# Kernel optimization log

Measured on AMD Instinct MI355X. Metric: run time of the kernel, lower is better.

The kernel has to match this reference:

```python
import jax, jax.numpy as jnp
import numpy as np

# ---- fixed wavelet filters (Selesnick FSfarras first-stage + Kingsbury Q-shift) ----
_F1 = np.array([
    [0.0, 0.0],
    [-0.08838834764832, -0.01122679215254],
    [0.08838834764832, 0.01122679215254],
    [0.69587998903400, 0.08838834764832],
    [0.69587998903400, 0.08838834764832],
    [0.08838834764832, -0.69587998903400],
    [-0.08838834764832, 0.69587998903400],
    [0.01122679215254, -0.08838834764832],
    [0.01122679215254, -0.08838834764832],
    [0.0, 0.0]], np.float32)
_F2 = np.array([
    [0.01122679215254, 0.0],
    [0.01122679215254, 0.0],
    [-0.08838834764832, -0.08838834764832],
    [0.08838834764832, -0.08838834764832],
    [0.69587998903400, 0.69587998903400],
    [0.69587998903400, -0.69587998903400],
    [0.08838834764832, 0.08838834764832],
    [-0.08838834764832, 0.08838834764832],
    [0.0, 0.01122679215254],
    [0.0, -0.01122679215254]], np.float32)
_Q1 = np.array([
    [0.03516384, 0.0],
    [0.0, 0.0],
    [-0.08832942, -0.11430184],
    [0.23389032, 0.0],
    [0.76027237, 0.58751830],
    [0.58751830, -0.76027237],
    [0.0, 0.23389032],
    [-0.11430184, 0.08832942],
    [0.0, 0.0],
    [0.0, -0.03516384]], np.float32)
_Q2 = np.array([
    [0.0, -0.03516384],
    [0.0, 0.0],
    [-0.11430184, 0.08832942],
    [0.0, 0.23389032],
    [0.58751830, -0.76027237],
    [0.76027237, 0.58751830],
    [0.23389032, 0.0],
    [-0.08832942, -0.11430184],
    [0.0, 0.0],
    [0.03516384, 0.0]], np.float32)
# synthesis filters are the time-reversed analysis filters
FSF = jnp.asarray(np.stack([_F1[::-1].copy(), _F2[::-1].copy()]))  # [2, 10, 2] first stage
SF = jnp.asarray(np.stack([_Q1[::-1].copy(), _Q2[::-1].copy()]))   # [2, 10, 2] Q-shift


def _upconv(x, f, axis):
    """Upsample-by-2 + full convolution with 1D filter f along `axis` (upfirdn(x,f,2,1))."""
    L = f.shape[0]
    xm = jnp.moveaxis(x, axis, -1)
    shp = xm.shape
    xr = xm.reshape(-1, 1, shp[-1])  # [M, 1, n] NCW
    k = f[::-1].astype(x.dtype).reshape(1, 1, L)  # flip -> true convolution
    y = jax.lax.conv_general_dilated(
        xr, k, window_strides=(1,), padding=[(L - 1, L - 1)],
        lhs_dilation=(2,), dimension_numbers=('NCW', 'OIW', 'NCW'))  # [M,1,2n+L-2]
    y = y.reshape(shp[:-1] + (y.shape[-1],))
    return jnp.moveaxis(y, -1, axis)


def sfb1d(lo, hi, sf, axis):
    """1D synthesis filter bank with periodic wrap + circular shift (Selesnick sfb1D)."""
    L = sf.shape[0]
    N = 2 * lo.shape[axis]
    y = _upconv(lo, sf[:, 0], axis) + _upconv(hi, sf[:, 1], axis)  # length N+L-2
    yN = jax.lax.slice_in_dim(y, 0, N, axis=axis)
    tail = jax.lax.slice_in_dim(y, N, N + L - 2, axis=axis)
    head = jax.lax.slice_in_dim(yN, 0, L - 2, axis=axis) + tail
    rest = jax.lax.slice_in_dim(yN, L - 2, N, axis=axis)
    return jnp.roll(jnp.concatenate([head, rest], axis=axis), 1 - L // 2, axis=axis)


def sfb2d(lo, hi3, sf_row, sf_col):
    """2D separable synthesis: hi3 = (LH, HL, HH); x is [B, H, W, C]."""
    lo = sfb1d(lo, hi3[0], sf_col, axis=2)
    h = sfb1d(hi3[1], hi3[2], sf_col, axis=2)
    return sfb1d(lo, h, sf_row, axis=1)


def _idtcwt(highs0, highs1, lows):
    inv_sqrt2 = jnp.asarray(1.0 / np.sqrt(2.0), highs0.dtype)

    def pm(a, b):
        return (a + b) * inv_sqrt2, (a - b) * inv_sqrt2

    # orientation butterflies per level (add_sub)
    wi = [[[[None] * 3 for _ in range(2)] for _ in range(2)] for _ in range(2)]
    for j, hj in enumerate((highs0, highs1)):
        for b in range(3):
            u, v = pm(hj[0, 0, b], hj[1, 1, b])
            wi[j][0][0][b], wi[j][1][1][b] = u, v
            u, v = pm(hj[0, 1, b], hj[1, 0, b])
            wi[j][0][1][b], wi[j][1][0][b] = u, v

    y = jnp.zeros_like(lows[0, 0], shape=(lows.shape[2], lows.shape[3] * 4,
                                          lows.shape[4] * 4, lows.shape[5]))
    for m in range(2):
        for n in range(2):
            lo = lows[m, n]
            lo = sfb2d(lo, wi[1][m][n], SF[m], SF[n])      # level 2 (Q-shift)
            lo = sfb2d(lo, wi[0][m][n], FSF[m], FSF[n])    # level 1 (first stage)
            y = y + lo
    return y / 2


def setup_inputs() -> dict:
    key = jax.random.key(0)
    k0, k1, k2 = jax.random.split(key, 3)
    B, C = 16, 3
    highs0 = jax.random.normal(k0, (2, 2, 3, B, 256, 256, C), dtype=jnp.float32)
    highs1 = jax.random.normal(k1, (2, 2, 3, B, 128, 128, C), dtype=jnp.float32)
    lows = jax.random.normal(k2, (2, 2, B, 128, 128, C), dtype=jnp.float32)
    return {"highs0": highs0, "highs1": highs1, "lows": lows}


def reference(highs0, highs1, lows):
    return _idtcwt(highs0, highs1, lows)
```

## Files before the change

### kernel.cpp

```cpp
#include <hip/hip_runtime.h>

#define INV_SQRT2 0.70710678118654752440f

__constant__ float c_first[2][10][2] = {
  { { 0.00000000000000f,  0.00000000000000f},
    {-0.08838834764832f, -0.01122679215254f},
    { 0.08838834764832f,  0.01122679215254f},
    { 0.69587998903400f,  0.08838834764832f},
    { 0.69587998903400f,  0.08838834764832f},
    { 0.08838834764832f, -0.69587998903400f},
    {-0.08838834764832f,  0.69587998903400f},
    { 0.01122679215254f, -0.08838834764832f},
    { 0.01122679215254f, -0.08838834764832f},
    { 0.00000000000000f,  0.00000000000000f} },
  { { 0.01122679215254f,  0.00000000000000f},
    { 0.01122679215254f,  0.00000000000000f},
    {-0.08838834764832f, -0.08838834764832f},
    { 0.08838834764832f, -0.08838834764832f},
    { 0.69587998903400f,  0.69587998903400f},
    { 0.69587998903400f, -0.69587998903400f},
    { 0.08838834764832f,  0.08838834764832f},
    {-0.08838834764832f,  0.08838834764832f},
    { 0.00000000000000f,  0.01122679215254f},
    { 0.00000000000000f, -0.01122679215254f} }
};

__constant__ float c_qshift[2][10][2] = {
  { { 0.03516384f,  0.00000000f},
    { 0.00000000f,  0.00000000f},
    {-0.08832942f, -0.11430184f},
    { 0.23389032f,  0.00000000f},
    { 0.76027237f,  0.58751830f},
    { 0.58751830f, -0.76027237f},
    { 0.00000000f,  0.23389032f},
    {-0.11430184f,  0.08832942f},
    { 0.00000000f,  0.00000000f},
    { 0.00000000f, -0.03516384f} },
  { { 0.00000000f, -0.03516384f},
    { 0.00000000f,  0.00000000f},
    {-0.11430184f,  0.08832942f},
    { 0.00000000f,  0.23389032f},
    { 0.58751830f, -0.76027237f},
    { 0.76027237f,  0.58751830f},
    { 0.23389032f,  0.00000000f},
    {-0.08832942f, -0.11430184f},
    { 0.00000000f,  0.00000000f},
    { 0.03516384f,  0.00000000f} }
};

__global__ __launch_bounds__(128) void idtcwt_stage1(
    const float* __restrict__ lows, const float* __restrict__ highs1,
    float* __restrict__ lo2)
{
  constexpr int HIN = 128, WIN = 128, C = 3, B = 16;
  constexpr int ROWF  = WIN * C;
  constexpr int ROWO  = 2 * WIN * C;
  constexpr int PLANE = HIN * WIN * C;
  constexpr int SEG   = 16;

  const int jj = blockIdx.x * 128 + threadIdx.x;
  const int c  = jj % 3;
  const int t  = jj / 3;
  const int z  = blockIdx.z;
  const int combo = z >> 4;
  const int b     = z & 15;
  const int m = combo >> 1, n = combo & 1;

  const float* lo = lows + (combo * B + b) * PLANE;
  const int pa = (m == n) ? 0 : 1;
  const int pb = (m == n) ? 3 : 2;
  const float sgn = (m == 0) ? 1.0f : -1.0f;
  const int bandStride = B * PLANE;
  const float* hA = highs1 + (pa * 3 * B + b) * PLANE;
  const float* hB = highs1 + (pb * 3 * B + b) * PLANE;

  int wc3[5];
#pragma unroll
  for (int p = 0; p < 5; ++p) {
    int w = t + 2 - p;
    if (w >= WIN) w -= WIN;
    if (w < 0)  w += WIN;
    wc3[p] = w * C + c;
  }

  float lae[5], lao[5], hae[5], hao[5];
#pragma unroll
  for (int k = 0; k < 5; ++k) { lae[k]=0.f; lao[k]=0.f; hae[k]=0.f; hao[k]=0.f; }

  const int s0 = blockIdx.y * SEG;
  float* outp = lo2 + (combo * B + b) * (4 * PLANE);

#pragma unroll 1
  for (int ui = 0; ui < SEG + 4; ++ui) {
    const int u  = (s0 - 2 + ui) & (HIN - 1);
#pragma unroll
    for (int k = 0; k < 4; ++k) { lae[k]=lae[k+1]; lao[k]=lao[k+1]; hae[k]=hae[k+1]; hao[k]=hao[k+1]; }
    const int rb = u * ROWF;

    float rl[5], rA[3][5], rB[3][5];
#pragma unroll
    for (int p = 0; p < 5; ++p) {
      const int idx = rb + wc3[p];
      rl[p]    = lo[idx];
      rA[0][p] = hA[idx];
      rB[0][p] = hB[idx];
      rA[1][p] = hA[idx +   bandStride];
      rB[1][p] = hB[idx +   bandStride];
      rA[2][p] = hA[idx + 2*bandStride];
      rB[2][p] = hB[idx + 2*bandStride];
    }

    float aLe=0.f, aLo=0.f, aHe=0.f, aHo=0.f;
#pragma unroll
    for (int p = 0; p < 5; ++p) {
      const float lv  = rl[p];
      const float lhv = (rA[0][p] + sgn * rB[0][p]) * INV_SQRT2;
      const float hlv = (rA[1][p] + sgn * rB[1][p]) * INV_SQRT2;
      const float hhv = (rA[2][p] + sgn * rB[2][p]) * INV_SQRT2;
      const float ce0 = c_qshift[n][9 - 2*p][0], ce1 = c_qshift[n][9 - 2*p][1];
      const float co0 = c_qshift[n][8 - 2*p][0], co1 = c_qshift[n][8 - 2*p][1];
      aLe += ce0 * lv  + ce1 * lhv;
      aLo += co0 * lv  + co1 * lhv;
      aHe += ce0 * hlv + ce1 * hhv;
      aHo += co0 * hlv + co1 * hhv;
    }
    lae[4]=aLe; lao[4]=aLo; hae[4]=aHe; hao[4]=aHo;

    if (ui >= 4) {
      const int s = s0 + ui - 4;
      float o00=0.f, o01=0.f, o10=0.f, o11=0.f;
#pragma unroll
      for (int p = 0; p < 5; ++p) {
        const float f0l = c_qshift[m][9 - 2*p][0], f0h = c_qshift[m][9 - 2*p][1];
        const float f1l = c_qshift[m][8 - 2*p][0], f1h = c_qshift[m][8 - 2*p][1];
        o00 += f0l*lae[4-p] + f0h*hae[4-p];
        o01 += f0l*lao[4-p] + f0h*hao[4-p];
        o10 += f1l*lae[4-p] + f1h*hae[4-p];
        o11 += f1l*lao[4-p] + f1h*hao[4-p];
      }
      float* q = outp + (2*s) * ROWO + (2*t) * C + c;
      q[0]        = o00;
      q[C]        = o01;
      q[ROWO]     = o10;
      q[ROWO + C] = o11;
    }
  }
}

__global__ __launch_bounds__(256, 3) void idtcwt_stage2(
    const float* __restrict__ lo2, const float* __restrict__ highs0,
    float* __restrict__ out)
{
  constexpr int HIN = 256, WIN = 256, C = 3, B = 16;
  constexpr int ROWF  = WIN * C;
  constexpr int ROWO  = 2 * WIN * C;
  constexpr int PLANE = HIN * WIN * C;
  constexpr int OPLANE = 512 * 512 * C;
  constexpr int SEG   = 16;
  constexpr int NI    = SEG + 4;
  constexpr int PITCH = 5;
  constexpr int BUFV4 = 272 * PITCH;

  __shared__ float4 lds4[2 * BUFV4];

  const int tid = threadIdx.x;
  const int jj  = blockIdx.x * 256 + tid;
  const int c   = jj % 3;
  const int t   = jj / 3;
  const int b   = blockIdx.z;

  const int bandStride = B * PLANE;
  const float* a0  = lo2 + (0 * B + b) * PLANE;
  const float* a1  = lo2 + (1 * B + b) * PLANE;
  const float* a2  = lo2 + (2 * B + b) * PLANE;
  const float* a3  = lo2 + (3 * B + b) * PLANE;
  const float* h00b0 = highs0 + (0 * 3 * B + b) * PLANE;
  const float* h01b0 = highs0 + (1 * 3 * B + b) * PLANE;
  const float* h10b0 = highs0 + (2 * 3 * B + b) * PLANE;
  const float* h11b0 = highs0 + (3 * 3 * B + b) * PLANE;
  const float* h00b1 = h00b0 + bandStride;
  const float* h01b1 = h01b0 + bandStride;
  const float* h10b1 = h10b0 + bandStride;
  const float* h11b1 = h11b0 + bandStride;
  const float* h00b2 = h00b0 + 2*bandStride;
  const float* h01b2 = h01b0 + 2*bandStride;
  const float* h10b2 = h10b0 + 2*bandStride;
  const float* h11b2 = h11b0 + 2*bandStride;

  int j1 = jj - 6;   if (j1 < 0)     j1 += ROWF;
  int j2 = jj + 250; if (j2 >= ROWF) j2 -= ROWF;
  const bool halo = (tid < 12);

  float wla0e[5], wla0o[5], wla1e[5], wla1o[5];
  float wha0e[5], wha0o[5], wha1e[5], wha1o[5];

  const int s0 = blockIdx.y * SEG;
  float* outb = out + b * OPLANE;

  float4 G0, G1, G2, G3, Hh0, Hh1, Hh2, Hh3;

#define S2_LOAD(I)                                                           \
  {                                                                          \
    const int rb_ = ((s0 - 2 + (I)) & (HIN - 1)) * ROWF;                     \
    const int o1_ = rb_ + j1;                                                \
    G0 = make_float4(a0[o1_], a1[o1_], a2[o1_], a3[o1_]);                    \
    G1 = make_float4(h00b0[o1_], h11b0[o1_], h01b0[o1_], h10b0[o1_]);        \
    G2 = make_float4(h00b1[o1_], h11b1[o1_], h01b1[o1_], h10b1[o1_]);        \
    G3 = make_float4(h00b2[o1_], h11b2[o1_], h01b2[o1_], h10b2[o1_]);        \
    if (halo) {                                                              \
      const int o2_ = rb_ + j2;                                              \
      Hh0 = make_float4(a0[o2_], a1[o2_], a2[o2_], a3[o2_]);                 \
      Hh1 = make_float4(h00b0[o2_], h11b0[o2_], h01b0[o2_], h10b0[o2_]);     \
      Hh2 = make_float4(h00b1[o2_], h11b1[o2_], h01b1[o2_], h10b1[o2_]);     \
      Hh3 = make_float4(h00b2[o2_], h11b2[o2_], h01b2[o2_], h10b2[o2_]);     \
    }                                                                        \
  }

#define S2_WRITE(DST)                                                        \
  {                                                                          \
    float4* w_ = (DST) + tid * PITCH;                                        \
    w_[0] = G0; w_[1] = G1; w_[2] = G2; w_[3] = G3;                          \
    if (halo) {                                                              \
      float4* w2_ = (DST) + (256 + tid) * PITCH;                             \
      w2_[0] = Hh0; w2_[1] = Hh1; w2_[2] = Hh2; w2_[3] = Hh3;                \
    }                                                                        \
  }

  float4* cur = lds4;
  float4* nxt = lds4 + BUFV4;

  S2_LOAD(0);
  S2_WRITE(cur);
  __syncthreads();

#pragma unroll 1
  for (int uo = 0; uo < 4; ++uo) {
#pragma unroll
    for (int k = 0; k < 5; ++k) {
      const int i = uo * 5 + k;

      if (i < NI - 1) {
        S2_LOAD(i + 1);
        __builtin_amdgcn_sched_barrier(0);
      }

      float A0e=0.f,A0o=0.f,A1e=0.f,A1o=0.f, H0e=0.f,H0o=0.f,H1e=0.f,H1o=0.f;
#pragma unroll
      for (int p = 0; p < 5; ++p) {
        const float4* qp = cur + (tid + (12 - 3*p)) * PITCH;
        const float4 q0 = qp[0], q1 = qp[1], q2 = qp[2], q3 = qp[3];
        const float a0e = c_first[0][9-2*p][0], a0o = c_first[0][8-2*p][0];
        const float b0e = c_first[0][9-2*p][1], b0o = c_first[0][8-2*p][1];
        const float a1e = c_first[1][9-2*p][0], a1o = c_first[1][8-2*p][0];
        const float b1e = c_first[1][9-2*p][1], b1o = c_first[1][8-2*p][1];
        {
          A0e += a0e*q0.x + a1e*q0.y;   A0o += a0o*q0.x + a1o*q0.y;
          A1e += a0e*q0.z + a1e*q0.w;   A1o += a0o*q0.z + a1o*q0.w;
        }
        {
          const float s1=(q1.x+q1.y)*INV_SQRT2, d1=(q1.x-q1.y)*INV_SQRT2;
          const float s2=(q1.z+q1.w)*INV_SQRT2, d2=(q1.z-q1.w)*INV_SQRT2;
          A0e += b0e*s1 + b1e*s2;   A0o += b0o*s1 + b1o*s2;
          A1e += b0e*d2 + b1e*d1;   A1o += b0o*d2 + b1o*d1;
        }
        {
          const float s1=(q2.x+q2.y)*INV_SQRT2, d1=(q2.x-q2.y)*INV_SQRT2;
          const float s2=(q2.z+q2.w)*INV_SQRT2, d2=(q2.z-q2.w)*INV_SQRT2;
          H0e += a0e*s1 + a1e*s2;   H0o += a0o*s1 + a1o*s2;
          H1e += a0e*d2 + a1e*d1;   H1o += a0o*d2 + a1o*d1;
        }
        {
          const float s1=(q3.x+q3.y)*INV_SQRT2, d1=(q3.x-q3.y)*INV_SQRT2;
          const float s2=(q3.z+q3.w)*INV_SQRT2, d2=(q3.z-q3.w)*INV_SQRT2;
          H0e += b0e*s1 + b1e*s2;   H0o += b0o*s1 + b1o*s2;
          H1e += b0e*d2 + b1e*d1;   H1o += b0o*d2 + b1o*d1;
        }
      }
      wla0e[k]=A0e; wla0o[k]=A0o; wla1e[k]=A1e; wla1o[k]=A1o;
      wha0e[k]=H0e; wha0o[k]=H0o; wha1e[k]=H1e; wha1o[k]=H1o;

      if (i >= 4) {
        const int s = s0 + i - 4;
        float o00=0.f, o01=0.f, o10=0.f, o11=0.f;
#pragma unroll
        for (int p = 0; p < 5; ++p) {
          const int kk = (k - p + 5) % 5;
          const float f00 = c_first[0][9-2*p][0], g00 = c_first[0][9-2*p][1];
          const float f01 = c_first[0][8-2*p][0], g01 = c_first[0][8-2*p][1];
          const float f10 = c_first[1][9-2*p][0], g10 = c_first[1][9-2*p][1];
          const float f11 = c_first[1][8-2*p][0], g11 = c_first[1][8-2*p][1];
          o00 += f00*wla0e[kk] + g00*wha0e[kk] + f10*wla1e[kk] + g10*wha1e[kk];
          o01 += f00*wla0o[kk] + g00*wha0o[kk] + f10*wla1o[kk] + g10*wha1o[kk];
          o10 += f01*wla0e[kk] + g01*wha0e[kk] + f11*wla1e[kk] + g11*wha1e[kk];
          o11 += f01*wla0o[kk] + g01*wha0o[kk] + f11*wla1o[kk] + g11*wha1o[kk];
        }
        float* q = outb + (2*s) * ROWO + (2*t) * C + c;
        q[0]        = o00 * 0.5f;
        q[C]        = o01 * 0.5f;
        q[ROWO]     = o10 * 0.5f;
        q[ROWO + C] = o11 * 0.5f;
      }

      if (i < NI - 1) {
        S2_WRITE(nxt);
      }
      __syncthreads();
      { float4* tmp = cur; cur = nxt; nxt = tmp; }
    }
  }
#undef S2_LOAD
#undef S2_WRITE
}

extern "C" void kernel_launch(void* const* d_in, const int* in_sizes, int n_in,
                              void* d_out, int out_size, void* d_ws, size_t ws_size,
                              hipStream_t stream) {
  const float* highs0 = (const float*)d_in[0];
  const float* highs1 = (const float*)d_in[1];
  const float* lows   = (const float*)d_in[2];
  float* out = (float*)d_out;
  float* lo2 = (float*)d_ws;

  dim3 b1(128), g1(3, 8, 64);
  hipLaunchKernelGGL(idtcwt_stage1, g1, b1, 0, stream, lows, highs1, lo2);

  dim3 b2(256), g2(3, 16, 16);
  hipLaunchKernelGGL(idtcwt_stage2, g2, b2, 0, stream, lo2, highs0, out);
}
```

Baseline: 112.4 us.

## Deepen stage-2 global prefetch to two rows and precombine sums into LDS

Stage 2 now keeps two register sets of global loads in flight, prefetching row I+2 while row I is computed. The row written to LDS is row I+1, which was loaded one phase earlier. The butterfly sums and differences and the scaling by 1/sqrt(2)*0.5 are applied once at LDS write time, so the five taps that read the values no longer redo them. The rolling 5-row window becomes a shift register instead of modular indexing. This aims to hide global load latency and cut ALU work, at the cost of more registers (possible lower occupancy) and extra register moves for the shift.

```diff
diff --git a/kernel.cpp b/kernel.cpp
--- a/kernel.cpp
+++ b/kernel.cpp
@@ -1,6 +1,7 @@
 #include <hip/hip_runtime.h>
 
 #define INV_SQRT2 0.70710678118654752440f
+#define KH 0.35355339059327376220f
 
 __constant__ float c_first[2][10][2] = {
   { { 0.00000000000000f,  0.00000000000000f},
@@ -193,123 +194,134 @@
 
   float wla0e[5], wla0o[5], wla1e[5], wla1o[5];
   float wha0e[5], wha0o[5], wha1e[5], wha1o[5];
+#pragma unroll
+  for (int k = 0; k < 5; ++k) {
+    wla0e[k]=0.f; wla0o[k]=0.f; wla1e[k]=0.f; wla1o[k]=0.f;
+    wha0e[k]=0.f; wha0o[k]=0.f; wha1e[k]=0.f; wha1o[k]=0.f;
+  }
 
   const int s0 = blockIdx.y * SEG;
   float* outb = out + b * OPLANE;
 
-  float4 G0, G1, G2, G3, Hh0, Hh1, Hh2, Hh3;
-
-#define S2_LOAD(I)                                                           \
-  {                                                                          \
-    const int rb_ = ((s0 - 2 + (I)) & (HIN - 1)) * ROWF;                     \
-    const int o1_ = rb_ + j1;                                                \
-    G0 = make_float4(a0[o1_], a1[o1_], a2[o1_], a3[o1_]);                    \
-    G1 = make_float4(h00b0[o1_], h11b0[o1_], h01b0[o1_], h10b0[o1_]);        \
-    G2 = make_float4(h00b1[o1_], h11b1[o1_], h01b1[o1_], h10b1[o1_]);        \
-    G3 = make_float4(h00b2[o1_], h11b2[o1_], h01b2[o1_], h10b2[o1_]);        \
-    if (halo) {                                                              \
-      const int o2_ = rb_ + j2;                                              \
-      Hh0 = make_float4(a0[o2_], a1[o2_], a2[o2_], a3[o2_]);                 \
-      Hh1 = make_float4(h00b0[o2_], h11b0[o2_], h01b0[o2_], h10b0[o2_]);     \
-      Hh2 = make_float4(h00b1[o2_], h11b1[o2_], h01b1[o2_], h10b1[o2_]);     \
-      Hh3 = make_float4(h00b2[o2_], h11b2[o2_], h01b2[o2_], h10b2[o2_]);     \
-    }                                                                        \
-  }
-
-#define S2_WRITE(DST)                                                        \
-  {                                                                          \
-    float4* w_ = (DST) + tid * PITCH;                                        \
-    w_[0] = G0; w_[1] = G1; w_[2] = G2; w_[3] = G3;                          \
-    if (halo) {                                                              \
-      float4* w2_ = (DST) + (256 + tid) * PITCH;                             \
-      w2_[0] = Hh0; w2_[1] = Hh1; w2_[2] = Hh2; w2_[3] = Hh3;                \
-    }                                                                        \
-  }
+  float4 GA0,GA1,GA2,GA3, HA0,HA1,HA2,HA3;
+  float4 GB0,GB1,GB2,GB3, HB0,HB1,HB2,HB3;
+
+  auto LOADR = [&](int I, float4& g0, float4& g1, float4& g2, float4& g3,
+                          float4& h0, float4& h1, float4& h2, float4& h3) {
+    const int rb = ((s0 - 2 + I) & (HIN - 1)) * ROWF;
+    const int o1 = rb + j1;
+    g0 = make_float4(a0[o1], a1[o1], a2[o1], a3[o1]);
+    g1 = make_float4(h00b0[o1], h11b0[o1], h01b0[o1], h10b0[o1]);
+    g2 = make_float4(h00b1[o1], h11b1[o1], h01b1[o1], h10b1[o1]);
+    g3 = make_float4(h00b2[o1], h11b2[o1], h01b2[o1], h10b2[o1]);
+    if (halo) {
+      const int o2 = rb + j2;
+      h0 = make_float4(a0[o2], a1[o2], a2[o2], a3[o2]);
+      h1 = make_float4(h00b0[o2], h11b0[o2], h01b0[o2], h10b0[o2]);
+      h2 = make_float4(h00b1[o2], h11b1[o2], h01b1[o2], h10b1[o2]);
+      h3 = make_float4(h00b2[o2], h11b2[o2], h01b2[o2], h10b2[o2]);
+    }
+  };
+
+  auto WRITER = [&](float4* dst,
+                    const float4& g0, const float4& g1, const float4& g2, const float4& g3,
+                    const float4& h0, const float4& h1, const float4& h2, const float4& h3) {
+    float4* wp = dst + tid * PITCH;
+    wp[0] = make_float4(g0.x*0.5f, g0.y*0.5f, g0.z*0.5f, g0.w*0.5f);
+    wp[1] = make_float4((g1.x+g1.y)*KH, (g1.x-g1.y)*KH, (g1.z+g1.w)*KH, (g1.z-g1.w)*KH);
+    wp[2] = make_float4((g2.x+g2.y)*KH, (g2.x-g2.y)*KH, (g2.z+g2.w)*KH, (g2.z-g2.w)*KH);
+    wp[3] = make_float4((g3.x+g3.y)*KH, (g3.x-g3.y)*KH, (g3.z+g3.w)*KH, (g3.z-g3.w)*KH);
+    if (halo) {
+      float4* wq = dst + (256 + tid) * PITCH;
+      wq[0] = make_float4(h0.x*0.5f, h0.y*0.5f, h0.z*0.5f, h0.w*0.5f);
+      wq[1] = make_float4((h1.x+h1.y)*KH, (h1.x-h1.y)*KH, (h1.z+h1.w)*KH, (h1.z-h1.w)*KH);
+      wq[2] = make_float4((h2.x+h2.y)*KH, (h2.x-h2.y)*KH, (h2.z+h2.w)*KH, (h2.z-h2.w)*KH);
+      wq[3] = make_float4((h3.x+h3.y)*KH, (h3.x-h3.y)*KH, (h3.z+h3.w)*KH, (h3.z-h3.w)*KH);
+    }
+  };
+
+  auto PHASE = [&](int I, const float4* cur) {
+    float A0e=0.f,A0o=0.f,A1e=0.f,A1o=0.f, H0e=0.f,H0o=0.f,H1e=0.f,H1o=0.f;
+#pragma unroll
+    for (int p = 0; p < 5; ++p) {
+      const float4* qp = cur + (tid + (12 - 3*p)) * PITCH;
+      const float4 q0 = qp[0], q1 = qp[1], q2 = qp[2], q3 = qp[3];
+      const float a0e = c_first[0][9-2*p][0], a0o = c_first[0][8-2*p][0];
+      const float b0e = c_first[0][9-2*p][1], b0o = c_first[0][8-2*p][1];
+      const float a1e = c_first[1][9-2*p][0], a1o = c_first[1][8-2*p][0];
+      const float b1e = c_first[1][9-2*p][1], b1o = c_first[1][8-2*p][1];
+      A0e += a0e*q0.x + a1e*q0.y;   A0o += a0o*q0.x + a1o*q0.y;
+      A1e += a0e*q0.z + a1e*q0.w;   A1o += a0o*q0.z + a1o*q0.w;
+      A0e += b0e*q1.x + b1e*q1.z;   A0o += b0o*q1.x + b1o*q1.z;
+      A1e += b0e*q1.w + b1e*q1.y;   A1o += b0o*q1.w + b1o*q1.y;
+      H0e += a0e*q2.x + a1e*q2.z;   H0o += a0o*q2.x + a1o*q2.z;
+      H1e += a0e*q2.w + a1e*q2.y;   H1o += a0o*q2.w + a1o*q2.y;
+      H0e += b0e*q3.x + b1e*q3.z;   H0o += b0o*q3.x + b1o*q3.z;
+      H1e += b0e*q3.w + b1e*q3.y;   H1o += b0o*q3.w + b1o*q3.y;
+    }
+#pragma unroll
+    for (int k = 0; k < 4; ++k) {
+      wla0e[k]=wla0e[k+1]; wla0o[k]=wla0o[k+1]; wla1e[k]=wla1e[k+1]; wla1o[k]=wla1o[k+1];
+      wha0e[k]=wha0e[k+1]; wha0o[k]=wha0o[k+1]; wha1e[k]=wha1e[k+1]; wha1o[k]=wha1o[k+1];
+    }
+    wla0e[4]=A0e; wla0o[4]=A0o; wla1e[4]=A1e; wla1o[4]=A1o;
+    wha0e[4]=H0e; wha0o[4]=H0o; wha1e[4]=H1e; wha1o[4]=H1o;
+
+    if (I >= 4) {
+      const int s = s0 + I - 4;
+      float o00=0.f, o01=0.f, o10=0.f, o11=0.f;
+#pragma unroll
+      for (int p = 0; p < 5; ++p) {
+        const float f00 = c_first[0][9-2*p][0], g00 = c_first[0][9-2*p][1];
+        const float f01 = c_first[0][8-2*p][0], g01 = c_first[0][8-2*p][1];
+        const float f10 = c_first[1][9-2*p][0], g10 = c_first[1][9-2*p][1];
+        const float f11 = c_first[1][8-2*p][0], g11 = c_first[1][8-2*p][1];
+        o00 += f00*wla0e[4-p] + g00*wha0e[4-p] + f10*wla1e[4-p] + g10*wha1e[4-p];
+        o01 += f00*wla0o[4-p] + g00*wha0o[4-p] + f10*wla1o[4-p] + g10*wha1o[4-p];
+        o10 += f01*wla0e[4-p] + g01*wha0e[4-p] + f11*wla1e[4-p] + g11*wha1e[4-p];
+        o11 += f01*wla0o[4-p] + g01*wha0o[4-p] + f11*wla1o[4-p] + g11*wha1o[4-p];
+      }
+      float* q = outb + (2*s) * ROWO + (2*t) * C + c;
+      q[0]        = o00;
+      q[C]        = o01;
+      q[ROWO]     = o10;
+      q[ROWO + C] = o11;
+    }
+  };
 
   float4* cur = lds4;
   float4* nxt = lds4 + BUFV4;
 
-  S2_LOAD(0);
-  S2_WRITE(cur);
+  LOADR(0, GA0,GA1,GA2,GA3, HA0,HA1,HA2,HA3);
+  LOADR(1, GB0,GB1,GB2,GB3, HB0,HB1,HB2,HB3);
+  WRITER(cur, GA0,GA1,GA2,GA3, HA0,HA1,HA2,HA3);
   __syncthreads();
 
 #pragma unroll 1
-  for (int uo = 0; uo < 4; ++uo) {
-#pragma unroll
-    for (int k = 0; k < 5; ++k) {
-      const int i = uo * 5 + k;
-
-      if (i < NI - 1) {
-        S2_LOAD(i + 1);
+  for (int io = 0; io < NI/2; ++io) {
+    {
+      const int I = 2*io;
+      if (I + 2 < NI) {
+        LOADR(I+2, GA0,GA1,GA2,GA3, HA0,HA1,HA2,HA3);
         __builtin_amdgcn_sched_barrier(0);
       }
-
-      float A0e=0.f,A0o=0.f,A1e=0.f,A1o=0.f, H0e=0.f,H0o=0.f,H1e=0.f,H1o=0.f;
-#pragma unroll
-      for (int p = 0; p < 5; ++p) {
-        const float4* qp = cur + (tid + (12 - 3*p)) * PITCH;
-        const float4 q0 = qp[0], q1 = qp[1], q2 = qp[2], q3 = qp[3];
-        const float a0e = c_first[0][9-2*p][0], a0o = c_first[0][8-2*p][0];
-        const float b0e = c_first[0][9-2*p][1], b0o = c_first[0][8-2*p][1];
-        const float a1e = c_first[1][9-2*p][0], a1o = c_first[1][8-2*p][0];
-        const float b1e = c_first[1][9-2*p][1], b1o = c_first[1][8-2*p][1];
-        {
-          A0e += a0e*q0.x + a1e*q0.y;   A0o += a0o*q0.x + a1o*q0.y;
-          A1e += a0e*q0.z + a1e*q0.w;   A1o += a0o*q0.z + a1o*q0.w;
-        }
-        {
-          const float s1=(q1.x+q1.y)*INV_SQRT2, d1=(q1.x-q1.y)*INV_SQRT2;
-          const float s2=(q1.z+q1.w)*INV_SQRT2, d2=(q1.z-q1.w)*INV_SQRT2;
-          A0e += b0e*s1 + b1e*s2;   A0o += b0o*s1 + b1o*s2;
-          A1e += b0e*d2 + b1e*d1;   A1o += b0o*d2 + b1o*d1;
-        }
-        {
-          const float s1=(q2.x+q2.y)*INV_SQRT2, d1=(q2.x-q2.y)*INV_SQRT2;
-          const float s2=(q2.z+q2.w)*INV_SQRT2, d2=(q2.z-q2.w)*INV_SQRT2;
-          H0e += a0e*s1 + a1e*s2;   H0o += a0o*s1 + a1o*s2;
-          H1e += a0e*d2 + a1e*d1;   H1o += a0o*d2 + a1o*d1;
-        }
-        {
-          const float s1=(q3.x+q3.y)*INV_SQRT2, d1=(q3.x-q3.y)*INV_SQRT2;
-          const float s2=(q3.z+q3.w)*INV_SQRT2, d2=(q3.z-q3.w)*INV_SQRT2;
-          H0e += b0e*s1 + b1e*s2;   H0o += b0o*s1 + b1o*s2;
-          H1e += b0e*d2 + b1e*d1;   H1o += b0o*d2 + b1o*d1;
-        }
+      PHASE(I, cur);
+      if (I + 1 < NI) WRITER(nxt, GB0,GB1,GB2,GB3, HB0,HB1,HB2,HB3);
+      __syncthreads();
+      float4* tmp = cur; cur = nxt; nxt = tmp;
+    }
+    {
+      const int I = 2*io + 1;
+      if (I + 2 < NI) {
+        LOADR(I+2, GB0,GB1,GB2,GB3, HB0,HB1,HB2,HB3);
+        __builtin_amdgcn_sched_barrier(0);
       }
-      wla0e[k]=A0e; wla0o[k]=A0o; wla1e[k]=A1e; wla1o[k]=A1o;
-      wha0e[k]=H0e; wha0o[k]=H0o; wha1e[k]=H1e; wha1o[k]=H1o;
-
-      if (i >= 4) {
-        const int s = s0 + i - 4;
-        float o00=0.f, o01=0.f, o10=0.f, o11=0.f;
-#pragma unroll
-        for (int p = 0; p < 5; ++p) {
-          const int kk = (k - p + 5) % 5;
-          const float f00 = c_first[0][9-2*p][0], g00 = c_first[0][9-2*p][1];
-          const float f01 = c_first[0][8-2*p][0], g01 = c_first[0][8-2*p][1];
-          const float f10 = c_first[1][9-2*p][0], g10 = c_first[1][9-2*p][1];
-          const float f11 = c_first[1][8-2*p][0], g11 = c_first[1][8-2*p][1];
-          o00 += f00*wla0e[kk] + g00*wha0e[kk] + f10*wla1e[kk] + g10*wha1e[kk];
-          o01 += f00*wla0o[kk] + g00*wha0o[kk] + f10*wla1o[kk] + g10*wha1o[kk];
-          o10 += f01*wla0e[kk] + g01*wha0e[kk] + f11*wla1e[kk] + g11*wha1e[kk];
-          o11 += f01*wla0o[kk] + g01*wha0o[kk] + f11*wla1o[kk] + g11*wha1o[kk];
-        }
-        float* q = outb + (2*s) * ROWO + (2*t) * C + c;
-        q[0]        = o00 * 0.5f;
-        q[C]        = o01 * 0.5f;
-        q[ROWO]     = o10 * 0.5f;
-        q[ROWO + C] = o11 * 0.5f;
-      }
-
-      if (i < NI - 1) {
-        S2_WRITE(nxt);
-      }
+      PHASE(I, cur);
+      if (I + 1 < NI) WRITER(nxt, GA0,GA1,GA2,GA3, HA0,HA1,HA2,HA3);
       __syncthreads();
-      { float4* tmp = cur; cur = nxt; nxt = tmp; }
+      float4* tmp = cur; cur = nxt; nxt = tmp;
     }
   }
-#undef S2_LOAD
-#undef S2_WRITE
 }
 
 extern "C" void kernel_launch(void* const* d_in, const int* in_sizes, int n_in,
```

New measurement: 183.7 us. +63.5%, slower.
